# Performance work log

Hardware: AMD Instinct MI355X
Metric: run time of the kernel (lower is better)

Reference implementation:

```python
import jax, jax.numpy as jnp
import numpy as np

BETA = 0.0  # vcon_steps=0 -> beta=0 -> pure MAM (max+min) path


def setup_inputs() -> dict:
    key = jax.random.key(0)
    k1, k2, k3 = jax.random.split(key, 3)
    in_features, out_features, tokens = 1024, 512, 256
    x = jax.random.normal(k1, (tokens, in_features), dtype=jnp.float32)
    # torch stores weight as [out_features, in_features]
    weight = jax.random.normal(k2, (out_features, in_features), dtype=jnp.float32) * (1.0 / np.sqrt(in_features))
    bias = jax.random.normal(k3, (out_features,), dtype=jnp.float32) * 0.02
    return {"x": x, "weight": weight, "bias": bias}


def reference(x, weight, bias):
    # w: [K, N] as in the kernel (weight.T)
    w = weight.T
    # elementwise-product tensor [B, K, N]; kernel fuses this with online max/min
    prod = x[:, :, None] * w[None, :, :]
    mam = jnp.max(prod, axis=1) + jnp.min(prod, axis=1)  # [B, N]
    if BETA > 0.0:
        lin = jnp.matmul(x, w)
        out = BETA * lin + (1.0 - BETA) * mam + bias
    else:
        out = mam + bias
    return out
```

## Files before the change

### kernel.cpp

```cpp
#include <hip/hip_runtime.h>
#include <float.h>

#define B_TOK 256
#define N_OUT 512
#define K_IN  1024

#define KSPLIT 8
#define KC     (K_IN / KSPLIT)
#define BT     16
#define NT     64

__global__ __launch_bounds__(256)
void mam_stage1(const float* __restrict__ x, const float* __restrict__ w,
                float* __restrict__ pmx, float* __restrict__ pmn) {
    __shared__ float ws[NT * KC];

    const int tid = threadIdx.x;
    const int b0  = blockIdx.x * BT;
    const int n0  = blockIdx.y * NT;
    const int kc  = blockIdx.z * KC;

    {
        const int r  = tid >> 2;
        const int cb = tid & 3;
        const float* gsrc = w + (size_t)(n0 + r) * K_IN + kc;
#pragma unroll
        for (int j = 0; j < 8; ++j) {
            const int c = cb + 4 * j;
            const float4 v = *reinterpret_cast<const float4*>(gsrc + c * 4);
            *reinterpret_cast<float4*>(&ws[r * KC + ((c ^ (r & 7)) << 2)]) = v;
        }
    }
    __syncthreads();

    const int wv = __builtin_amdgcn_readfirstlane(tid >> 6);
    const int ln = tid & 63;
    const float* xb0 = x + (size_t)(b0 + wv * 4 + 0) * K_IN + kc;
    const float* xb1 = x + (size_t)(b0 + wv * 4 + 1) * K_IN + kc;
    const float* xb2 = x + (size_t)(b0 + wv * 4 + 2) * K_IN + kc;
    const float* xb3 = x + (size_t)(b0 + wv * 4 + 3) * K_IN + kc;

    float mx0 = -FLT_MAX, mx1 = -FLT_MAX, mx2 = -FLT_MAX, mx3 = -FLT_MAX;
    float mn0 =  FLT_MAX, mn1 =  FLT_MAX, mn2 =  FLT_MAX, mn3 =  FLT_MAX;

    const int swz = ln & 7;
#pragma unroll 4
    for (int c = 0; c < KC / 4; ++c) {
        const float4 wk = *reinterpret_cast<const float4*>(
            &ws[ln * KC + ((c ^ swz) << 2)]);
        const float4 x0 = *reinterpret_cast<const float4*>(xb0 + c * 4);
        const float4 x1 = *reinterpret_cast<const float4*>(xb1 + c * 4);
        const float4 x2 = *reinterpret_cast<const float4*>(xb2 + c * 4);
        const float4 x3 = *reinterpret_cast<const float4*>(xb3 + c * 4);

        {   const float p0 = x0.x * wk.x, p1 = x0.y * wk.y, p2 = x0.z * wk.z, p3 = x0.w * wk.w;
            mx0 = fmaxf(fmaxf(mx0, p0), p1); mx0 = fmaxf(fmaxf(mx0, p2), p3);
            mn0 = fminf(fminf(mn0, p0), p1); mn0 = fminf(fminf(mn0, p2), p3); }
        {   const float p0 = x1.x * wk.x, p1 = x1.y * wk.y, p2 = x1.z * wk.z, p3 = x1.w * wk.w;
            mx1 = fmaxf(fmaxf(mx1, p0), p1); mx1 = fmaxf(fmaxf(mx1, p2), p3);
            mn1 = fminf(fminf(mn1, p0), p1); mn1 = fminf(fminf(mn1, p2), p3); }
        {   const float p0 = x2.x * wk.x, p1 = x2.y * wk.y, p2 = x2.z * wk.z, p3 = x2.w * wk.w;
            mx2 = fmaxf(fmaxf(mx2, p0), p1); mx2 = fmaxf(fmaxf(mx2, p2), p3);
            mn2 = fminf(fminf(mn2, p0), p1); mn2 = fminf(fminf(mn2, p2), p3); }
        {   const float p0 = x3.x * wk.x, p1 = x3.y * wk.y, p2 = x3.z * wk.z, p3 = x3.w * wk.w;
            mx3 = fmaxf(fmaxf(mx3, p0), p1); mx3 = fmaxf(fmaxf(mx3, p2), p3);
            mn3 = fminf(fminf(mn3, p0), p1); mn3 = fminf(fminf(mn3, p2), p3); }
    }

    const size_t plane = (size_t)B_TOK * N_OUT;
    const size_t base  = (size_t)blockIdx.z * plane
                       + (size_t)(b0 + wv * 4) * N_OUT + n0 + ln;
    pmx[base + 0 * N_OUT] = mx0;  pmn[base + 0 * N_OUT] = mn0;
    pmx[base + 1 * N_OUT] = mx1;  pmn[base + 1 * N_OUT] = mn1;
    pmx[base + 2 * N_OUT] = mx2;  pmn[base + 2 * N_OUT] = mn2;
    pmx[base + 3 * N_OUT] = mx3;  pmn[base + 3 * N_OUT] = mn3;
}

__global__ __launch_bounds__(256)
void mam_stage2(const float* __restrict__ pmx, const float* __restrict__ pmn,
                const float* __restrict__ bias, float* __restrict__ out) {
    const size_t i4 = ((size_t)blockIdx.x * 256 + threadIdx.x) * 4;
    const size_t plane = (size_t)B_TOK * N_OUT;
    float4 MX = *reinterpret_cast<const float4*>(pmx + i4);
    float4 MN = *reinterpret_cast<const float4*>(pmn + i4);
#pragma unroll
    for (int p = 1; p < KSPLIT; ++p) {
        const float4 a = *reinterpret_cast<const float4*>(pmx + (size_t)p * plane + i4);
        const float4 i = *reinterpret_cast<const float4*>(pmn + (size_t)p * plane + i4);
        MX.x = fmaxf(MX.x, a.x); MX.y = fmaxf(MX.y, a.y);
        MX.z = fmaxf(MX.z, a.z); MX.w = fmaxf(MX.w, a.w);
        MN.x = fminf(MN.x, i.x); MN.y = fminf(MN.y, i.y);
        MN.z = fminf(MN.z, i.z); MN.w = fminf(MN.w, i.w);
    }
    const float4 bb = *reinterpret_cast<const float4*>(bias + (i4 & (N_OUT - 1)));
    float4 o;
    o.x = MX.x + MN.x + bb.x; o.y = MX.y + MN.y + bb.y;
    o.z = MX.z + MN.z + bb.z; o.w = MX.w + MN.w + bb.w;
    *reinterpret_cast<float4*>(out + i4) = o;
}

__global__ __launch_bounds__(256)
void mam_simple(const float* __restrict__ x, const float* __restrict__ w,
                const float* __restrict__ bias, float* __restrict__ out) {
    const int idx = blockIdx.x * 256 + threadIdx.x;
    const int b = idx / N_OUT, n = idx % N_OUT;
    const float* xr = x + (size_t)b * K_IN;
    const float* wr = w + (size_t)n * K_IN;
    float mx = -FLT_MAX, mn = FLT_MAX;
#pragma unroll 4
    for (int k = 0; k < K_IN; k += 4) {
        const float4 xv = *reinterpret_cast<const float4*>(xr + k);
        const float4 wv = *reinterpret_cast<const float4*>(wr + k);
        const float p0 = xv.x * wv.x, p1 = xv.y * wv.y;
        const float p2 = xv.z * wv.z, p3 = xv.w * wv.w;
        mx = fmaxf(fmaxf(mx, p0), p1);
        mx = fmaxf(fmaxf(mx, p2), p3);
        mn = fminf(fminf(mn, p0), p1);
        mn = fminf(fminf(mn, p2), p3);
    }
    out[idx] = mx + mn + bias[n];
}

extern "C" void kernel_launch(void* const* d_in, const int* in_sizes, int n_in,
                              void* d_out, int out_size, void* d_ws, size_t ws_size,
                              hipStream_t stream) {
    const float* x    = (const float*)d_in[0];
    const float* w    = (const float*)d_in[1];
    const float* bias = (const float*)d_in[2];
    float* out = (float*)d_out;

    const size_t plane = (size_t)B_TOK * N_OUT;
    const size_t need  = 2 * (size_t)KSPLIT * plane * sizeof(float);

    if (ws_size >= need) {
        float* pmx = (float*)d_ws;
        float* pmn = pmx + (size_t)KSPLIT * plane;
        mam_stage1<<<dim3(B_TOK / BT, N_OUT / NT, KSPLIT), 256, 0, stream>>>(x, w, pmx, pmn);
        mam_stage2<<<(int)(plane / 4 / 256), 256, 0, stream>>>(pmx, pmn, bias, out);
    } else {
        mam_simple<<<(B_TOK * N_OUT) / 256, 256, 0, stream>>>(x, w, bias, out);
    }
}
```

Measured before the change: 19.58 us.

## Use 4x4 register tiles with x staged in LDS and intra-block K split

Stage1 now loads both the w tile and the x tile into swizzled shared memory. Each thread computes a 4x4 (token x output) register tile, and each of the four waves covers a quarter of the block's K chunk. The per-wave partial max/min results are then reduced through shared memory and written with float4 stores. The aim is more arithmetic per LDS load and no repeated global x loads, at the cost of an extra reduction pass, two more barriers and more registers.

```diff
diff --git a/kernel.cpp b/kernel.cpp
--- a/kernel.cpp
+++ b/kernel.cpp
@@ -6,74 +6,122 @@
 #define K_IN  1024
 
 #define KSPLIT 8
-#define KC     (K_IN / KSPLIT)
+#define KT     (K_IN / KSPLIT)
 #define BT     16
 #define NT     64
 
 __global__ __launch_bounds__(256)
 void mam_stage1(const float* __restrict__ x, const float* __restrict__ w,
                 float* __restrict__ pmx, float* __restrict__ pmn) {
-    __shared__ float ws[NT * KC];
+    __shared__ float lds[10240];
+    float* ws = lds;
+    float* xs = lds + 8192;
 
     const int tid = threadIdx.x;
+    const int wv  = tid >> 6;
+    const int ln  = tid & 63;
     const int b0  = blockIdx.x * BT;
     const int n0  = blockIdx.y * NT;
-    const int kc  = blockIdx.z * KC;
+    const int kc  = blockIdx.z * KT;
 
     {
-        const int r  = tid >> 2;
-        const int cb = tid & 3;
-        const float* gsrc = w + (size_t)(n0 + r) * K_IN + kc;
+        const int cb = ln & 15;
+        const int u  = ln >> 4;
 #pragma unroll
-        for (int j = 0; j < 8; ++j) {
-            const int c = cb + 4 * j;
-            const float4 v = *reinterpret_cast<const float4*>(gsrc + c * 4);
-            *reinterpret_cast<float4*>(&ws[r * KC + ((c ^ (r & 7)) << 2)]) = v;
+        for (int p = 0; p < 4; ++p) {
+            const int r = 16 * wv + 4 * p + u;
+            const int q = r >> 2;
+            const float* src = w + (size_t)(n0 + r) * K_IN + kc;
+#pragma unroll
+            for (int m = 0; m < 2; ++m) {
+                const int c = cb + 16 * m;
+                const float4 v = *reinterpret_cast<const float4*>(src + c * 4);
+                *reinterpret_cast<float4*>(&ws[r * 128 + ((c ^ q) << 2)]) = v;
+            }
+        }
+    }
+    {
+        const int cb = ln & 15;
+        const int u  = ln >> 4;
+        const int b  = 4 * wv + u;
+        const float* src = x + (size_t)(b0 + b) * K_IN + kc;
+#pragma unroll
+        for (int m = 0; m < 2; ++m) {
+            const int c = cb + 16 * m;
+            const float4 v = *reinterpret_cast<const float4*>(src + c * 4);
+            *reinterpret_cast<float4*>(&xs[b * 128 + ((c ^ b) << 2)]) = v;
         }
     }
     __syncthreads();
 
-    const int wv = __builtin_amdgcn_readfirstlane(tid >> 6);
-    const int ln = tid & 63;
-    const float* xb0 = x + (size_t)(b0 + wv * 4 + 0) * K_IN + kc;
-    const float* xb1 = x + (size_t)(b0 + wv * 4 + 1) * K_IN + kc;
-    const float* xb2 = x + (size_t)(b0 + wv * 4 + 2) * K_IN + kc;
-    const float* xb3 = x + (size_t)(b0 + wv * 4 + 3) * K_IN + kc;
+    const int nq = ln & 15;
+    const int bq = ln >> 4;
 
-    float mx0 = -FLT_MAX, mx1 = -FLT_MAX, mx2 = -FLT_MAX, mx3 = -FLT_MAX;
-    float mn0 =  FLT_MAX, mn1 =  FLT_MAX, mn2 =  FLT_MAX, mn3 =  FLT_MAX;
+    float mx[4][4], mn[4][4];
+#pragma unroll
+    for (int i = 0; i < 4; ++i)
+#pragma unroll
+        for (int j = 0; j < 4; ++j) { mx[i][j] = -FLT_MAX; mn[i][j] = FLT_MAX; }
 
-    const int swz = ln & 7;
-#pragma unroll 4
-    for (int c = 0; c < KC / 4; ++c) {
-        const float4 wk = *reinterpret_cast<const float4*>(
-            &ws[ln * KC + ((c ^ swz) << 2)]);
-        const float4 x0 = *reinterpret_cast<const float4*>(xb0 + c * 4);
-        const float4 x1 = *reinterpret_cast<const float4*>(xb1 + c * 4);
-        const float4 x2 = *reinterpret_cast<const float4*>(xb2 + c * 4);
-        const float4 x3 = *reinterpret_cast<const float4*>(xb3 + c * 4);
+#pragma unroll 2
+    for (int cl = 0; cl < 8; ++cl) {
+        const int c = 8 * wv + cl;
+        float4 wf[4], xf[4];
+#pragma unroll
+        for (int j = 0; j < 4; ++j)
+            wf[j] = *reinterpret_cast<const float4*>(
+                &ws[(4 * nq + j) * 128 + ((c ^ nq) << 2)]);
+#pragma unroll
+        for (int i = 0; i < 4; ++i)
+            xf[i] = *reinterpret_cast<const float4*>(
+                &xs[(4 * bq + i) * 128 + ((c ^ (4 * bq + i)) << 2)]);
 
-        {   const float p0 = x0.x * wk.x, p1 = x0.y * wk.y, p2 = x0.z * wk.z, p3 = x0.w * wk.w;
-            mx0 = fmaxf(fmaxf(mx0, p0), p1); mx0 = fmaxf(fmaxf(mx0, p2), p3);
-            mn0 = fminf(fminf(mn0, p0), p1); mn0 = fminf(fminf(mn0, p2), p3); }
-        {   const float p0 = x1.x * wk.x, p1 = x1.y * wk.y, p2 = x1.z * wk.z, p3 = x1.w * wk.w;
-            mx1 = fmaxf(fmaxf(mx1, p0), p1); mx1 = fmaxf(fmaxf(mx1, p2), p3);
-            mn1 = fminf(fminf(mn1, p0), p1); mn1 = fminf(fminf(mn1, p2), p3); }
-        {   const float p0 = x2.x * wk.x, p1 = x2.y * wk.y, p2 = x2.z * wk.z, p3 = x2.w * wk.w;
-            mx2 = fmaxf(fmaxf(mx2, p0), p1); mx2 = fmaxf(fmaxf(mx2, p2), p3);
-            mn2 = fminf(fminf(mn2, p0), p1); mn2 = fminf(fminf(mn2, p2), p3); }
-        {   const float p0 = x3.x * wk.x, p1 = x3.y * wk.y, p2 = x3.z * wk.z, p3 = x3.w * wk.w;
-            mx3 = fmaxf(fmaxf(mx3, p0), p1); mx3 = fmaxf(fmaxf(mx3, p2), p3);
-            mn3 = fminf(fminf(mn3, p0), p1); mn3 = fminf(fminf(mn3, p2), p3); }
+#pragma unroll
+        for (int i = 0; i < 4; ++i) {
+#pragma unroll
+            for (int j = 0; j < 4; ++j) {
+                const float p0 = xf[i].x * wf[j].x;
+                const float p1 = xf[i].y * wf[j].y;
+                const float p2 = xf[i].z * wf[j].z;
+                const float p3 = xf[i].w * wf[j].w;
+                mx[i][j] = fmaxf(fmaxf(mx[i][j], p0), p1);
+                mx[i][j] = fmaxf(fmaxf(mx[i][j], p2), p3);
+                mn[i][j] = fminf(fminf(mn[i][j], p0), p1);
+                mn[i][j] = fminf(fminf(mn[i][j], p2), p3);
+            }
+        }
     }
 
-    const size_t plane = (size_t)B_TOK * N_OUT;
-    const size_t base  = (size_t)blockIdx.z * plane
-                       + (size_t)(b0 + wv * 4) * N_OUT + n0 + ln;
-    pmx[base + 0 * N_OUT] = mx0;  pmn[base + 0 * N_OUT] = mn0;
-    pmx[base + 1 * N_OUT] = mx1;  pmn[base + 1 * N_OUT] = mn1;
-    pmx[base + 2 * N_OUT] = mx2;  pmn[base + 2 * N_OUT] = mn2;
-    pmx[base + 3 * N_OUT] = mx3;  pmn[base + 3 * N_OUT] = mn3;
+    __syncthreads();
+    float* red = lds;
+#pragma unroll
+    for (int i = 0; i < 4; ++i) {
+        const int ol = (4 * bq + i) * 64 + 4 * nq;
+        float4 a = make_float4(mx[i][0], mx[i][1], mx[i][2], mx[i][3]);
+        float4 d = make_float4(mn[i][0], mn[i][1], mn[i][2], mn[i][3]);
+        *reinterpret_cast<float4*>(&red[(wv * 2 + 0) * 1024 + ol]) = a;
+        *reinterpret_cast<float4*>(&red[(wv * 2 + 1) * 1024 + ol]) = d;
+    }
+    __syncthreads();
+
+    {
+        float4 MX = *reinterpret_cast<const float4*>(&red[0 * 1024 + tid * 4]);
+        float4 MN = *reinterpret_cast<const float4*>(&red[1 * 1024 + tid * 4]);
+#pragma unroll
+        for (int v = 1; v < 4; ++v) {
+            const float4 a = *reinterpret_cast<const float4*>(&red[(v * 2 + 0) * 1024 + tid * 4]);
+            const float4 d = *reinterpret_cast<const float4*>(&red[(v * 2 + 1) * 1024 + tid * 4]);
+            MX.x = fmaxf(MX.x, a.x); MX.y = fmaxf(MX.y, a.y);
+            MX.z = fmaxf(MX.z, a.z); MX.w = fmaxf(MX.w, a.w);
+            MN.x = fminf(MN.x, d.x); MN.y = fminf(MN.y, d.y);
+            MN.z = fminf(MN.z, d.z); MN.w = fminf(MN.w, d.w);
+        }
+        const int bl = tid >> 4;
+        const int nl = (tid & 15) * 4;
+        const size_t o = ((size_t)blockIdx.z * B_TOK + b0 + bl) * N_OUT + n0 + nl;
+        *reinterpret_cast<float4*>(&pmx[o]) = MX;
+        *reinterpret_cast<float4*>(&pmn[o]) = MN;
+    }
 }
 
 __global__ __launch_bounds__(256)
@@ -86,11 +134,11 @@
 #pragma unroll
     for (int p = 1; p < KSPLIT; ++p) {
         const float4 a = *reinterpret_cast<const float4*>(pmx + (size_t)p * plane + i4);
-        const float4 i = *reinterpret_cast<const float4*>(pmn + (size_t)p * plane + i4);
+        const float4 d = *reinterpret_cast<const float4*>(pmn + (size_t)p * plane + i4);
         MX.x = fmaxf(MX.x, a.x); MX.y = fmaxf(MX.y, a.y);
         MX.z = fmaxf(MX.z, a.z); MX.w = fmaxf(MX.w, a.w);
-        MN.x = fminf(MN.x, i.x); MN.y = fminf(MN.y, i.y);
-        MN.z = fminf(MN.z, i.z); MN.w = fminf(MN.w, i.w);
+        MN.x = fminf(MN.x, d.x); MN.y = fminf(MN.y, d.y);
+        MN.z = fminf(MN.z, d.z); MN.w = fminf(MN.w, d.w);
     }
     const float4 bb = *reinterpret_cast<const float4*>(bias + (i4 & (N_OUT - 1)));
     float4 o;
```

After: 20.92 us. +6.9%, slower.
